# Performance work log

Measured on AMD Instinct MI355X. Metric: run time of the kernel, lower is better.

## Reference

```python
import jax, jax.numpy as jnp
import numpy as np

HEADS = 4
C_HEAD = 32


def setup_inputs() -> dict:
    key = jax.random.key(0)
    k1, k2, k3 = jax.random.split(key, 3)
    c_in = 256
    c_hid = HEADS * C_HEAD  # 128
    x = jax.random.normal(k1, (4, c_in, 64, 64), dtype=jnp.float32)
    # 1x1 conv weights stored as [out, in]
    w_qkv = jax.random.normal(k2, (3 * c_hid, c_in), dtype=jnp.float32) * (c_in ** -0.5)
    w_out = jax.random.normal(k3, (c_in, c_hid), dtype=jnp.float32) * (c_hid ** -0.5)
    b_out = jnp.zeros((c_in,), dtype=jnp.float32)
    return {"x": x, "w_qkv": w_qkv, "w_out": w_out, "b_out": b_out}


def reference(x, w_qkv, w_out, b_out):
    b, c, h, w = x.shape
    scale = C_HEAD ** -0.5
    # 1x1 conv == channel matmul
    qkv = jnp.einsum('bchw,oc->bohw', x, w_qkv)  # [b, 3*c_hid, h, w]
    q, k, v = jnp.split(qkv, 3, axis=1)
    # b (heads c_head) x y -> b heads c_head (x y)
    def to_heads(t):
        return t.reshape(b, HEADS, C_HEAD, h * w)
    q, k, v = to_heads(q) * scale, to_heads(k), to_heads(v)
    sim = jnp.einsum('bhci,bhcj->bhij', q, k)  # [b, heads, N, N]
    sim = sim - jax.lax.stop_gradient(jnp.max(sim, axis=-1, keepdims=True))
    attn = jax.nn.softmax(sim, axis=-1)
    out = jnp.einsum('bhij,bhcj->bhic', attn, v)  # [b, heads, N, c_head]
    # b h (x y) c -> b (h c) x y
    out = out.transpose(0, 1, 3, 2).reshape(b, HEADS * C_HEAD, h, w)
    out = jnp.einsum('bchw,oc->bohw', out, w_out) + b_out[None, :, None, None]
    return out
```

## Files before the change

### kernel.cpp

```cpp
#include <hip/hip_runtime.h>
#include <hip/hip_bf16.h>
#include <cstdint>
#include <cstddef>


#define NB 4
#define CIN 256
#define CHID 128
#define HEADS 4
#define CHEAD 32
#define NPOS 4096
#define BH 16
#define NTOT 16384
#define QKV_O 384
#define QSCALE_LOG2E 0.2550348229f

typedef float f32x2 __attribute__((ext_vector_type(2)));
typedef float f32x4 __attribute__((ext_vector_type(4)));
typedef float f32x16 __attribute__((ext_vector_type(16)));
typedef short s16x8 __attribute__((ext_vector_type(8)));

static __device__ __forceinline__ unsigned short f2bf(float f) {
    union { float f; unsigned u; } v; v.f = f;
    unsigned r = v.u + 0x7FFFu + ((v.u >> 16) & 1u);
    return (unsigned short)(r >> 16);
}

static __device__ __forceinline__ unsigned int pk2bf(float a, float b) {
    union { __hip_bfloat162 h; unsigned int u; } c;
    c.h = __float22bfloat162_rn(float2{a, b});
    return c.u;
}

static __device__ __forceinline__ void plswap(unsigned& a, unsigned& b) {
#if __has_builtin(__builtin_amdgcn_permlane32_swap)
    auto r = __builtin_amdgcn_permlane32_swap((int)a, (int)b, false, false);
    a = (unsigned)r[0];
    b = (unsigned)r[1];
#else
    int hh = (threadIdx.x >> 5) & 1;
    unsigned ta = (unsigned)__shfl_xor((int)a, 32);
    unsigned tb = (unsigned)__shfl_xor((int)b, 32);
    unsigned na = hh ? tb : a;
    unsigned nb = hh ? b : ta;
    a = na; b = nb;
#endif
}

static __device__ __forceinline__ s16x8 mk8(unsigned a, unsigned b, unsigned c, unsigned d) {
    union { unsigned u[4]; s16x8 v; } x;
    x.u[0] = a; x.u[1] = b; x.u[2] = c; x.u[3] = d;
    return x.v;
}

static __device__ __forceinline__ void async_cp16(const void* g, void* l) {
    __builtin_amdgcn_global_load_lds((const __attribute__((address_space(1))) unsigned int*)g,
                                     (__attribute__((address_space(3))) unsigned int*)l, 16, 0, 0);
}

#define MFMA32(a, b, c) __builtin_amdgcn_mfma_f32_32x32x16_bf16(a, b, c, 0, 0, 0)


#define PTILES (NB * (CIN / 64) * (NPOS / 64))
__global__ __launch_bounds__(256) void k_prep(const float* __restrict__ x,
                                              unsigned short* __restrict__ xT,
                                              const float* __restrict__ wqkv,
                                              const float* __restrict__ wout,
                                              unsigned short* __restrict__ wqkv_bf,
                                              unsigned short* __restrict__ wout_bf) {
    if (blockIdx.x >= PTILES) {
        int i = (blockIdx.x - PTILES) * 256 + threadIdx.x;
        if (i < QKV_O * CIN) wqkv_bf[i] = f2bf(wqkv[i]);
        if (i < CIN * CHID)  wout_bf[i] = f2bf(wout[i]);
        return;
    }
    __shared__ float tile[64][65];
    const int per_b = (CIN / 64) * (NPOS / 64);
    int b   = blockIdx.x / per_b;
    int rem = blockIdx.x % per_b;
    int ct = rem / (NPOS / 64);
    int nt = rem % (NPOS / 64);
    int c0 = ct * 64, n0 = nt * 64;
    int t = threadIdx.x;
    const float* xb = x + (size_t)b * CIN * NPOS;
#pragma unroll
    for (int it = 0; it < 4; ++it) {
        int c  = (t >> 4) + it * 16;
        int n4 = (t & 15) * 4;
        f32x4 v = *(const f32x4*)(xb + (size_t)(c0 + c) * NPOS + n0 + n4);
        tile[c][n4] = v[0]; tile[c][n4 + 1] = v[1];
        tile[c][n4 + 2] = v[2]; tile[c][n4 + 3] = v[3];
    }
    __syncthreads();
    unsigned short* xTb = xT + (size_t)b * NPOS * CIN;
#pragma unroll
    for (int it = 0; it < 2; ++it) {
        int slot = it * 256 + t;
        int n  = slot >> 3;
        int c8 = (slot & 7) * 8;
        union { unsigned short u[8]; s16x8 v; } pk;
#pragma unroll
        for (int r = 0; r < 8; ++r) pk.u[r] = f2bf(tile[c8 + r][n]);
        *(s16x8*)(xTb + (size_t)(n0 + n) * CIN + c0 + c8) = pk.v;
    }
}

__global__ __launch_bounds__(256, 4) void k_qkv(const unsigned short* __restrict__ wq,
                                                const unsigned short* __restrict__ xT,
                                                unsigned short* __restrict__ Q,
                                                unsigned short* __restrict__ K,
                                                unsigned short* __restrict__ V) {
    __shared__ __align__(16) unsigned char smem[2 * 12288];
    int mt = blockIdx.x % 3;
    int nt = blockIdx.x / 3;
    int wid = threadIdx.x >> 6, lane = threadIdx.x & 63;
    int quad = lane >> 4, low4 = lane & 15;
    int o0 = mt * 128, n0 = nt * 64;
    int lb = lane * 16;

    const unsigned short* srcA0 = wq + (size_t)(o0 + wid * 32 + low4) * CIN + quad * 8;
    const unsigned short* srcA1 = srcA0 + 16 * CIN;
    const unsigned short* srcB  = xT + (size_t)(n0 + wid * 16 + low4) * CIN + quad * 8;
    int dA0 = wid * 2048, dA1 = dA0 + 1024, dB = 8192 + wid * 1024;

    async_cp16(srcA0, smem + dA0 + lb);
    async_cp16(srcA1, smem + dA1 + lb);
    async_cp16(srcB,  smem + dB  + lb);
    __syncthreads();

    f32x4 acc[2][4] = {};
    for (int c = 0; c < 8; ++c) {
        if (c < 7) {
            unsigned char* nxt = smem + ((c + 1) & 1) * 12288;
            async_cp16(srcA0 + (c + 1) * 32, nxt + dA0 + lb);
            async_cp16(srcA1 + (c + 1) * 32, nxt + dA1 + lb);
            async_cp16(srcB  + (c + 1) * 32, nxt + dB  + lb);
        }
        const unsigned char* cur = smem + (c & 1) * 12288;
        s16x8 a0 = *(const s16x8*)(cur + wid * 2048 + lb);
        s16x8 a1 = *(const s16x8*)(cur + wid * 2048 + 1024 + lb);
#pragma unroll
        for (int j = 0; j < 4; ++j) {
            s16x8 bj = *(const s16x8*)(cur + 8192 + j * 1024 + lb);
            acc[0][j] = __builtin_amdgcn_mfma_f32_16x16x32_bf16(a0, bj, acc[0][j], 0, 0, 0);
            acc[1][j] = __builtin_amdgcn_mfma_f32_16x16x32_bf16(a1, bj, acc[1][j], 0, 0, 0);
        }
        __syncthreads();
    }

    int b = n0 >> 12, nbase = n0 & 4095;
    if (mt < 2) {
        unsigned short (*vtT)[136] = (unsigned short(*)[136])smem;
        float sc = (mt == 0) ? QSCALE_LOG2E : 1.0f;
#pragma unroll
        for (int i = 0; i < 2; ++i) {
            int ob = wid * 32 + i * 16 + quad * 4;
#pragma unroll
            for (int j = 0; j < 4; ++j) {
                int nl = j * 16 + low4;
                f32x4 v = acc[i][j];
                unsigned long long d =
                    (unsigned long long)pk2bf(v[0] * sc, v[1] * sc) |
                    ((unsigned long long)pk2bf(v[2] * sc, v[3] * sc) << 32);
                *(unsigned long long*)(&vtT[nl][ob]) = d;
            }
        }
        __syncthreads();
        if (mt == 0) {
#pragma unroll
            for (int it = 0; it < 4; ++it) {
                int slot = it * 256 + threadIdx.x;
                int n = slot >> 4, c16 = slot & 15;
                s16x8 val = *(const s16x8*)(&vtT[n][c16 * 8]);
                int o = c16 * 8, head = o >> 5, ch = o & 31;
                *(s16x8*)(Q + ((size_t)(b * 4 + head) * NPOS + nbase + n) * 32 + ch) = val;
            }
        } else {
#pragma unroll
            for (int it = 0; it < 4; ++it) {
                int slot = it * 256 + threadIdx.x;
                int c16 = slot >> 6, n = slot & 63;
                s16x8 val = *(const s16x8*)(&vtT[n][c16 * 8]);
                int o = c16 * 8, head = o >> 5, c0h = o & 31;
                int f = c0h >> 4, hh = (c0h >> 3) & 1;
                int nG = nbase + n;
                int bh = b * 4 + head;
                size_t addr = (((size_t)bh * 128 + (nG >> 5)) * 2 + f) * 512
                            + (size_t)((((hh << 5) | (nG & 31)) << 3));
                *(s16x8*)(K + addr) = val;
            }
        }
    } else {
        unsigned short* vt = (unsigned short*)smem;
#pragma unroll
        for (int i = 0; i < 2; ++i) {
            int ol = wid * 32 + i * 16 + quad * 4;
#pragma unroll
            for (int j = 0; j < 4; ++j) {
                int col = j * 16 + low4;
#pragma unroll
                for (int r = 0; r < 4; ++r) vt[(ol + r) * 80 + col] = f2bf(acc[i][j][r]);
            }
        }
        __syncthreads();
#pragma unroll
        for (int rep = 0; rep < 4; ++rep) {
            int idx = rep * 256 + threadIdx.x;
            int row = idx >> 3, c8 = idx & 7;
            s16x8 val = *(const s16x8*)(vt + row * 80 + c8 * 8);
            int head = row >> 5, ch = row & 31;
            int bh = b * 4 + head;
            int nstart = nbase + c8 * 8;
            int kc = nstart >> 4, hh = (nstart >> 3) & 1;
            *(s16x8*)(V + ((size_t)(bh * 256 + kc) * 64 + ((hh << 5) | ch)) * 8) = val;
        }
    }
}

__global__ __launch_bounds__(256, 4) void k_attn(const unsigned short* __restrict__ Q,
                                                 const unsigned short* __restrict__ K,
                                                 const unsigned short* __restrict__ V,
                                                 unsigned short* __restrict__ attnO) {
    __shared__ __align__(16) unsigned char smem[2 * 16384];
    int bh = blockIdx.x & 15;
    int qt = blockIdx.x >> 4;
    int wid = threadIdx.x >> 6;
    int lane = threadIdx.x & 63;
    int q5 = lane & 31, h = lane >> 5;
    int qg = wid & 1, kh = wid >> 1;
    int q0 = qt * 64 + qg * 32;
    int khk = kh * 2048;

    const unsigned short* Qp = Q + (size_t)bh * NPOS * 32;

    s16x8 bq0 = *(const s16x8*)(Qp + (size_t)(q0 + q5) * 32 + h * 8);
    s16x8 bq1 = *(const s16x8*)(Qp + (size_t)(q0 + q5) * 32 + 16 + h * 8);

    const unsigned short* pKf = K + (size_t)bh * 131072 + lane * 8;
    const unsigned short* pVf = V + (size_t)bh * 131072 + lane * 8;

    auto stage = [&](int bufi, int k0) {
        unsigned char* wb = smem + bufi * 16384 + kh * 8192;
        if (qg == 0) {
            const unsigned short* p = pKf + (size_t)(k0 >> 5) * 1024;
            async_cp16(p,        wb);
            async_cp16(p + 512,  wb + 1024);
            async_cp16(p + 1024, wb + 2048);
            async_cp16(p + 1536, wb + 3072);
        } else {
            const unsigned short* p = pVf + (size_t)(k0 >> 4) * 512;
            async_cp16(p,        wb + 4096);
            async_cp16(p + 512,  wb + 5120);
            async_cp16(p + 1024, wb + 6144);
            async_cp16(p + 1536, wb + 7168);
        }
    };

    f32x16 oT = {};
    f32x2 lacc0 = {0.0f, 0.0f}, lacc1 = {0.0f, 0.0f};
    const int lby = lane * 16;

    stage(0, khk);

#pragma unroll 1
    for (int it = 0; it < 32; ++it) {
        if (it + 1 < 32) {
            stage((it + 1) & 1, khk + (it + 1) * 64);
            asm volatile("s_waitcnt vmcnt(4)" ::: "memory");
        } else {
            asm volatile("s_waitcnt vmcnt(0)" ::: "memory");
        }
        asm volatile("s_barrier" ::: "memory");

        const unsigned char* kb = smem + (it & 1) * 16384 + kh * 8192;
#pragma unroll
        for (int t = 0; t < 2; ++t) {
            s16x8 ak0 = *(const s16x8*)(kb + t * 2048 + lby);
            s16x8 ak1 = *(const s16x8*)(kb + t * 2048 + 1024 + lby);
            f32x16 s = {};
            __builtin_amdgcn_s_setprio(1);
            s = MFMA32(ak0, bq0, s);
            s = MFMA32(ak1, bq1, s);
            __builtin_amdgcn_s_setprio(0);
            unsigned p[8];
#pragma unroll
            for (int i = 0; i < 8; ++i) {
                float e0 = __builtin_amdgcn_exp2f(s[2 * i]);
                float e1 = __builtin_amdgcn_exp2f(s[2 * i + 1]);
                f32x2 e = {e0, e1};
                if (i & 1) lacc0 += e;
                else       lacc1 += e;
                p[i] = pk2bf(e0, e1);
            }
            plswap(p[0], p[2]); plswap(p[1], p[3]);
            plswap(p[4], p[6]); plswap(p[5], p[7]);
            s16x8 bplo = mk8(p[0], p[1], p[2], p[3]);
            s16x8 bphi = mk8(p[4], p[5], p[6], p[7]);

            s16x8 av0 = *(const s16x8*)(kb + 4096 + (2 * t) * 1024 + lby);
            s16x8 av1 = *(const s16x8*)(kb + 4096 + (2 * t + 1) * 1024 + lby);
            __builtin_amdgcn_s_setprio(1);
            oT = MFMA32(av0, bplo, oT);
            oT = MFMA32(av1, bphi, oT);
            __builtin_amdgcn_s_setprio(0);
        }
        asm volatile("s_barrier" ::: "memory");
    }

    float lsum = lacc0[0] + lacc0[1] + lacc1[0] + lacc1[1];
    lsum += __shfl_xor(lsum, 32);

    if (kh) {
        float* area = (float*)(smem + qg * 4352);
#pragma unroll
        for (int j = 0; j < 4; ++j)
            *(f32x4*)(area + j * 256 + lane * 4) =
                f32x4{oT[4 * j], oT[4 * j + 1], oT[4 * j + 2], oT[4 * j + 3]};
        area[1024 + lane] = lsum;
    }
    __syncthreads();
    if (!kh) {
        const float* area = (const float*)(smem + qg * 4352);
        lsum += area[1024 + lane];
        float inv = 1.0f / lsum;
        int b = bh >> 2, head = bh & 3;
        int n = q0 + q5;
        unsigned short* base = attnO + ((size_t)(b * NPOS + n)) * CHID + head * 32 + 4 * h;
#pragma unroll
        for (int j = 0; j < 4; ++j) {
            f32x4 r = *(const f32x4*)(area + j * 256 + lane * 4);
            unsigned long long d =
                (unsigned long long)pk2bf((oT[4 * j] + r[0]) * inv, (oT[4 * j + 1] + r[1]) * inv) |
                ((unsigned long long)pk2bf((oT[4 * j + 2] + r[2]) * inv, (oT[4 * j + 3] + r[3]) * inv) << 32);
            *(unsigned long long*)(base + 8 * j) = d;
        }
    }
}

__global__ __launch_bounds__(256, 4) void k_out(const unsigned short* __restrict__ wo,
                                                const unsigned short* __restrict__ attnO,
                                                const float* __restrict__ bias,
                                                float* __restrict__ out) {
    __shared__ __align__(16) unsigned char smem[2 * 12288];
    int mt = blockIdx.x & 1;
    int nt = blockIdx.x >> 1;
    int wid = threadIdx.x >> 6, lane = threadIdx.x & 63;
    int quad = lane >> 4, low4 = lane & 15;
    int o0 = mt * 128, n0 = nt * 64;
    int lb = lane * 16;

    const unsigned short* srcA0 = wo + (size_t)(o0 + wid * 32 + low4) * CHID + quad * 8;
    const unsigned short* srcA1 = srcA0 + 16 * CHID;
    const unsigned short* srcB  = attnO + (size_t)(n0 + wid * 16 + low4) * CHID + quad * 8;
    int dA0 = wid * 2048, dA1 = dA0 + 1024, dB = 8192 + wid * 1024;

    async_cp16(srcA0, smem + dA0 + lb);
    async_cp16(srcA1, smem + dA1 + lb);
    async_cp16(srcB,  smem + dB  + lb);
    __syncthreads();

    f32x4 acc[2][4] = {};
    for (int c = 0; c < 4; ++c) {
        if (c < 3) {
            unsigned char* nxt = smem + ((c + 1) & 1) * 12288;
            async_cp16(srcA0 + (c + 1) * 32, nxt + dA0 + lb);
            async_cp16(srcA1 + (c + 1) * 32, nxt + dA1 + lb);
            async_cp16(srcB  + (c + 1) * 32, nxt + dB  + lb);
        }
        const unsigned char* cur = smem + (c & 1) * 12288;
        s16x8 a0 = *(const s16x8*)(cur + wid * 2048 + lb);
        s16x8 a1 = *(const s16x8*)(cur + wid * 2048 + 1024 + lb);
#pragma unroll
        for (int j = 0; j < 4; ++j) {
            s16x8 bj = *(const s16x8*)(cur + 8192 + j * 1024 + lb);
            acc[0][j] = __builtin_amdgcn_mfma_f32_16x16x32_bf16(a0, bj, acc[0][j], 0, 0, 0);
            acc[1][j] = __builtin_amdgcn_mfma_f32_16x16x32_bf16(a1, bj, acc[1][j], 0, 0, 0);
        }
        __syncthreads();
    }

    float (*larea)[68] = (float(*)[68])smem;
    int b = n0 >> 12, nb = n0 & 4095;
#pragma unroll
    for (int half = 0; half < 2; ++half) {
        if ((wid >> 1) == half) {
#pragma unroll
            for (int i = 0; i < 2; ++i) {
                int row = (wid & 1) * 32 + i * 16 + quad * 4;
                int o = o0 + half * 64 + row;
#pragma unroll
                for (int j = 0; j < 4; ++j) {
                    int nl = j * 16 + low4;
#pragma unroll
                    for (int r = 0; r < 4; ++r)
                        larea[row + r][nl] = acc[i][j][r] + bias[o + r];
                }
            }
        }
        __syncthreads();
#pragma unroll
        for (int it = 0; it < 4; ++it) {
            int slot = it * 256 + threadIdx.x;
            int row = slot >> 4, nn4 = (slot & 15) * 4;
            int o = o0 + half * 64 + row;
            f32x4 v = *(const f32x4*)(&larea[row][nn4]);
            *(f32x4*)(out + ((size_t)(b * CIN + o)) * NPOS + nb + nn4) = v;
        }
        __syncthreads();
    }
}

extern "C" void kernel_launch(void* const* d_in, const int* in_sizes, int n_in,
                              void* d_out, int out_size, void* d_ws, size_t ws_size,
                              hipStream_t stream) {
    const float* x    = (const float*)d_in[0];
    const float* wqkv = (const float*)d_in[1];
    const float* wout = (const float*)d_in[2];
    const float* bout = (const float*)d_in[3];
    float* out = (float*)d_out;

    unsigned short* Q       = (unsigned short*)d_ws;
    unsigned short* K       = Q + (size_t)BH * NPOS * 32;
    unsigned short* V       = K + (size_t)BH * NPOS * 32;
    unsigned short* attnO   = V + (size_t)BH * 32 * NPOS;
    unsigned short* xT      = attnO + (size_t)NTOT * CHID;
    unsigned short* wqkv_bf = xT + (size_t)NTOT * CIN;
    unsigned short* wout_bf = wqkv_bf + QKV_O * CIN;

    k_prep<<<PTILES + (QKV_O * CIN + 255) / 256, 256, 0, stream>>>(x, xT, wqkv, wout, wqkv_bf, wout_bf);
    k_qkv<<<3 * (NTOT / 64), 256, 0, stream>>>(wqkv_bf, xT, Q, K, V);
    k_attn<<<(NPOS / 64) * BH, 256, 0, stream>>>(Q, K, V, attnO);
    k_out<<<2 * (NTOT / 64), 256, 0, stream>>>(wout_bf, attnO, bout, out);
}
```

Before: 157.0 us.

## Fuse attention and output projection into one 1024-thread kernel per query tile

Merges the attention kernel and the output 1x1 conv kernel. Each 1024-thread block now processes all four heads of one batch for a 64-query tile. The normalized attention output stays in LDS as a bf16 tile, which feeds the wout MFMA projection directly. This removes the global attnO write and re-read and one kernel launch. In exchange each block uses 128KB of LDS, the grid shrinks to 256 blocks, and the launch bound (1024, 4) may squeeze the register budget and cause spills in the attention loop.

```diff
diff --git a/kernel.cpp b/kernel.cpp
--- a/kernel.cpp
+++ b/kernel.cpp
@@ -217,22 +217,24 @@
     }
 }
 
-__global__ __launch_bounds__(256, 4) void k_attn(const unsigned short* __restrict__ Q,
-                                                 const unsigned short* __restrict__ K,
-                                                 const unsigned short* __restrict__ V,
-                                                 unsigned short* __restrict__ attnO) {
-    __shared__ __align__(16) unsigned char smem[2 * 16384];
-    int bh = blockIdx.x & 15;
-    int qt = blockIdx.x >> 4;
+__global__ __launch_bounds__(1024, 4) void k_attn_out(const unsigned short* __restrict__ Q,
+                                                      const unsigned short* __restrict__ K,
+                                                      const unsigned short* __restrict__ V,
+                                                      const unsigned short* __restrict__ wo,
+                                                      const float* __restrict__ bias,
+                                                      float* __restrict__ out) {
+    __shared__ __align__(16) unsigned char smem[131072];
+    int b  = blockIdx.x & 3;
+    int qt = blockIdx.x >> 2;
     int wid = threadIdx.x >> 6;
     int lane = threadIdx.x & 63;
     int q5 = lane & 31, h = lane >> 5;
-    int qg = wid & 1, kh = wid >> 1;
+    int head = wid >> 2, kh = (wid >> 1) & 1, qg = wid & 1;
+    int bh = b * 4 + head;
     int q0 = qt * 64 + qg * 32;
     int khk = kh * 2048;
 
     const unsigned short* Qp = Q + (size_t)bh * NPOS * 32;
-
     s16x8 bq0 = *(const s16x8*)(Qp + (size_t)(q0 + q5) * 32 + h * 8);
     s16x8 bq1 = *(const s16x8*)(Qp + (size_t)(q0 + q5) * 32 + 16 + h * 8);
 
@@ -240,7 +242,7 @@
     const unsigned short* pVf = V + (size_t)bh * 131072 + lane * 8;
 
     auto stage = [&](int bufi, int k0) {
-        unsigned char* wb = smem + bufi * 16384 + kh * 8192;
+        unsigned char* wb = smem + bufi * 65536 + head * 16384 + kh * 8192;
         if (qg == 0) {
             const unsigned short* p = pKf + (size_t)(k0 >> 5) * 1024;
             async_cp16(p,        wb);
@@ -272,7 +274,7 @@
         }
         asm volatile("s_barrier" ::: "memory");
 
-        const unsigned char* kb = smem + (it & 1) * 16384 + kh * 8192;
+        const unsigned char* kb = smem + (it & 1) * 65536 + head * 16384 + kh * 8192;
 #pragma unroll
         for (int t = 0; t < 2; ++t) {
             s16x8 ak0 = *(const s16x8*)(kb + t * 2048 + lby);
@@ -310,8 +312,9 @@
     float lsum = lacc0[0] + lacc0[1] + lacc1[0] + lacc1[1];
     lsum += __shfl_xor(lsum, 32);
 
+    float* area = (float*)(smem + (head * 2 + qg) * 4352);
+    unsigned short* oblk = (unsigned short*)(smem + 98304);
     if (kh) {
-        float* area = (float*)(smem + qg * 4352);
 #pragma unroll
         for (int j = 0; j < 4; ++j)
             *(f32x4*)(area + j * 256 + lane * 4) =
@@ -320,93 +323,49 @@
     }
     __syncthreads();
     if (!kh) {
-        const float* area = (const float*)(smem + qg * 4352);
         lsum += area[1024 + lane];
         float inv = 1.0f / lsum;
-        int b = bh >> 2, head = bh & 3;
-        int n = q0 + q5;
-        unsigned short* base = attnO + ((size_t)(b * NPOS + n)) * CHID + head * 32 + 4 * h;
+        int n = qg * 32 + q5;
 #pragma unroll
         for (int j = 0; j < 4; ++j) {
             f32x4 r = *(const f32x4*)(area + j * 256 + lane * 4);
             unsigned long long d =
                 (unsigned long long)pk2bf((oT[4 * j] + r[0]) * inv, (oT[4 * j + 1] + r[1]) * inv) |
                 ((unsigned long long)pk2bf((oT[4 * j + 2] + r[2]) * inv, (oT[4 * j + 3] + r[3]) * inv) << 32);
-            *(unsigned long long*)(base + 8 * j) = d;
-        }
-    }
-}
-
-__global__ __launch_bounds__(256, 4) void k_out(const unsigned short* __restrict__ wo,
-                                                const unsigned short* __restrict__ attnO,
-                                                const float* __restrict__ bias,
-                                                float* __restrict__ out) {
-    __shared__ __align__(16) unsigned char smem[2 * 12288];
-    int mt = blockIdx.x & 1;
-    int nt = blockIdx.x >> 1;
-    int wid = threadIdx.x >> 6, lane = threadIdx.x & 63;
+            *(unsigned long long*)(oblk + n * 136 + head * 32 + 4 * h + 8 * j) = d;
+        }
+    }
+    __syncthreads();
+
     int quad = lane >> 4, low4 = lane & 15;
-    int o0 = mt * 128, n0 = nt * 64;
-    int lb = lane * 16;
-
-    const unsigned short* srcA0 = wo + (size_t)(o0 + wid * 32 + low4) * CHID + quad * 8;
-    const unsigned short* srcA1 = srcA0 + 16 * CHID;
-    const unsigned short* srcB  = attnO + (size_t)(n0 + wid * 16 + low4) * CHID + quad * 8;
-    int dA0 = wid * 2048, dA1 = dA0 + 1024, dB = 8192 + wid * 1024;
-
-    async_cp16(srcA0, smem + dA0 + lb);
-    async_cp16(srcA1, smem + dA1 + lb);
-    async_cp16(srcB,  smem + dB  + lb);
-    __syncthreads();
-
-    f32x4 acc[2][4] = {};
-    for (int c = 0; c < 4; ++c) {
-        if (c < 3) {
-            unsigned char* nxt = smem + ((c + 1) & 1) * 12288;
-            async_cp16(srcA0 + (c + 1) * 32, nxt + dA0 + lb);
-            async_cp16(srcA1 + (c + 1) * 32, nxt + dA1 + lb);
-            async_cp16(srcB  + (c + 1) * 32, nxt + dB  + lb);
-        }
-        const unsigned char* cur = smem + (c & 1) * 12288;
-        s16x8 a0 = *(const s16x8*)(cur + wid * 2048 + lb);
-        s16x8 a1 = *(const s16x8*)(cur + wid * 2048 + 1024 + lb);
+    const unsigned short* wrow = wo + (size_t)(wid * 16 + low4) * CHID + quad * 8;
+    s16x8 af[4];
+#pragma unroll
+    for (int c4 = 0; c4 < 4; ++c4) af[c4] = *(const s16x8*)(wrow + c4 * 32);
+    f32x4 acc[4] = {};
+#pragma unroll
+    for (int c4 = 0; c4 < 4; ++c4) {
 #pragma unroll
         for (int j = 0; j < 4; ++j) {
-            s16x8 bj = *(const s16x8*)(cur + 8192 + j * 1024 + lb);
-            acc[0][j] = __builtin_amdgcn_mfma_f32_16x16x32_bf16(a0, bj, acc[0][j], 0, 0, 0);
-            acc[1][j] = __builtin_amdgcn_mfma_f32_16x16x32_bf16(a1, bj, acc[1][j], 0, 0, 0);
-        }
-        __syncthreads();
-    }
-
-    float (*larea)[68] = (float(*)[68])smem;
-    int b = n0 >> 12, nb = n0 & 4095;
-#pragma unroll
-    for (int half = 0; half < 2; ++half) {
-        if ((wid >> 1) == half) {
-#pragma unroll
-            for (int i = 0; i < 2; ++i) {
-                int row = (wid & 1) * 32 + i * 16 + quad * 4;
-                int o = o0 + half * 64 + row;
-#pragma unroll
-                for (int j = 0; j < 4; ++j) {
-                    int nl = j * 16 + low4;
-#pragma unroll
-                    for (int r = 0; r < 4; ++r)
-                        larea[row + r][nl] = acc[i][j][r] + bias[o + r];
-                }
-            }
-        }
-        __syncthreads();
-#pragma unroll
-        for (int it = 0; it < 4; ++it) {
-            int slot = it * 256 + threadIdx.x;
-            int row = slot >> 4, nn4 = (slot & 15) * 4;
-            int o = o0 + half * 64 + row;
-            f32x4 v = *(const f32x4*)(&larea[row][nn4]);
-            *(f32x4*)(out + ((size_t)(b * CIN + o)) * NPOS + nb + nn4) = v;
-        }
-        __syncthreads();
+            s16x8 bj = *(const s16x8*)(oblk + (j * 16 + low4) * 136 + c4 * 32 + quad * 8);
+            acc[j] = __builtin_amdgcn_mfma_f32_16x16x32_bf16(af[c4], bj, acc[j], 0, 0, 0);
+        }
+    }
+
+    f32x4 bv = *(const f32x4*)(bias + wid * 16 + quad * 4);
+    float* larea = (float*)smem;
+#pragma unroll
+    for (int j = 0; j < 4; ++j)
+#pragma unroll
+        for (int r = 0; r < 4; ++r)
+            larea[(wid * 16 + quad * 4 + r) * 68 + j * 16 + low4] = acc[j][r] + bv[r];
+    __syncthreads();
+#pragma unroll
+    for (int it2 = 0; it2 < 4; ++it2) {
+        int slot = it2 * 1024 + threadIdx.x;
+        int row = slot >> 4, n4 = (slot & 15) * 4;
+        *(f32x4*)(out + ((size_t)(b * CIN + row)) * NPOS + qt * 64 + n4) =
+            *(const f32x4*)(larea + row * 68 + n4);
     }
 }
 
@@ -422,13 +381,11 @@
     unsigned short* Q       = (unsigned short*)d_ws;
     unsigned short* K       = Q + (size_t)BH * NPOS * 32;
     unsigned short* V       = K + (size_t)BH * NPOS * 32;
-    unsigned short* attnO   = V + (size_t)BH * 32 * NPOS;
-    unsigned short* xT      = attnO + (size_t)NTOT * CHID;
+    unsigned short* xT      = V + (size_t)BH * 32 * NPOS;
     unsigned short* wqkv_bf = xT + (size_t)NTOT * CIN;
     unsigned short* wout_bf = wqkv_bf + QKV_O * CIN;
 
     k_prep<<<PTILES + (QKV_O * CIN + 255) / 256, 256, 0, stream>>>(x, xT, wqkv, wout, wqkv_bf, wout_bf);
     k_qkv<<<3 * (NTOT / 64), 256, 0, stream>>>(wqkv_bf, xT, Q, K, V);
-    k_attn<<<(NPOS / 64) * BH, 256, 0, stream>>>(Q, K, V, attnO);
-    k_out<<<2 * (NTOT / 64), 256, 0, stream>>>(wout_bf, attnO, bout, out);
-}
+    k_attn_out<<<NB * (NPOS / 64), 1024, 0, stream>>>(Q, K, V, wout_bf, bout, out);
+}
```

After: 162.8 us. +3.7%, slower.

## Split attention keys across four waves per 32-query tile with per-wave staging

Applied to the files above, without the earlier changes.

Each block now handles 32 queries instead of 64. Its four waves each take a quarter of the keys, and each wave stages its own K/V chunk into a private LDS slice, so the per-iteration block barriers go away. The grid doubles, LDS per block halves and launch bounds allow 8 blocks per CU, all to raise occupancy. In exchange, each wave waits on its own loads with only single-buffering plus an issue-ahead after the LDS reads. The final reduction now merges three partial outputs through shared memory, and each K/V tile is loaded by twice as many blocks.

```diff
diff --git a/kernel.cpp b/kernel.cpp
--- a/kernel.cpp
+++ b/kernel.cpp
@@ -217,101 +217,86 @@
     }
 }
 
-__global__ __launch_bounds__(256, 4) void k_attn(const unsigned short* __restrict__ Q,
+__global__ __launch_bounds__(256, 8) void k_attn(const unsigned short* __restrict__ Q,
                                                  const unsigned short* __restrict__ K,
                                                  const unsigned short* __restrict__ V,
                                                  unsigned short* __restrict__ attnO) {
-    __shared__ __align__(16) unsigned char smem[2 * 16384];
+    __shared__ __align__(16) unsigned char smem[16384];
     int bh = blockIdx.x & 15;
     int qt = blockIdx.x >> 4;
     int wid = threadIdx.x >> 6;
     int lane = threadIdx.x & 63;
     int q5 = lane & 31, h = lane >> 5;
-    int qg = wid & 1, kh = wid >> 1;
-    int q0 = qt * 64 + qg * 32;
-    int khk = kh * 2048;
+    int q0 = qt * 32;
+    int k0 = wid * 1024;
 
     const unsigned short* Qp = Q + (size_t)bh * NPOS * 32;
-
     s16x8 bq0 = *(const s16x8*)(Qp + (size_t)(q0 + q5) * 32 + h * 8);
     s16x8 bq1 = *(const s16x8*)(Qp + (size_t)(q0 + q5) * 32 + 16 + h * 8);
 
     const unsigned short* pKf = K + (size_t)bh * 131072 + lane * 8;
     const unsigned short* pVf = V + (size_t)bh * 131072 + lane * 8;
-
-    auto stage = [&](int bufi, int k0) {
-        unsigned char* wb = smem + bufi * 16384 + kh * 8192;
-        if (qg == 0) {
-            const unsigned short* p = pKf + (size_t)(k0 >> 5) * 1024;
-            async_cp16(p,        wb);
-            async_cp16(p + 512,  wb + 1024);
-            async_cp16(p + 1024, wb + 2048);
-            async_cp16(p + 1536, wb + 3072);
-        } else {
-            const unsigned short* p = pVf + (size_t)(k0 >> 4) * 512;
-            async_cp16(p,        wb + 4096);
-            async_cp16(p + 512,  wb + 5120);
-            async_cp16(p + 1024, wb + 6144);
-            async_cp16(p + 1536, wb + 7168);
-        }
+    unsigned char* wb = smem + wid * 4096;
+    const int lby = lane * 16;
+
+    auto stage = [&](int kk) {
+        const unsigned short* pk = pKf + (size_t)(kk >> 5) * 1024;
+        const unsigned short* pv = pVf + (size_t)(kk >> 4) * 512;
+        async_cp16(pk,       wb);
+        async_cp16(pk + 512, wb + 1024);
+        async_cp16(pv,       wb + 2048);
+        async_cp16(pv + 512, wb + 3072);
     };
 
     f32x16 oT = {};
     f32x2 lacc0 = {0.0f, 0.0f}, lacc1 = {0.0f, 0.0f};
-    const int lby = lane * 16;
-
-    stage(0, khk);
+
+    stage(k0);
 
 #pragma unroll 1
     for (int it = 0; it < 32; ++it) {
-        if (it + 1 < 32) {
-            stage((it + 1) & 1, khk + (it + 1) * 64);
-            asm volatile("s_waitcnt vmcnt(4)" ::: "memory");
-        } else {
-            asm volatile("s_waitcnt vmcnt(0)" ::: "memory");
-        }
-        asm volatile("s_barrier" ::: "memory");
-
-        const unsigned char* kb = smem + (it & 1) * 16384 + kh * 8192;
-#pragma unroll
-        for (int t = 0; t < 2; ++t) {
-            s16x8 ak0 = *(const s16x8*)(kb + t * 2048 + lby);
-            s16x8 ak1 = *(const s16x8*)(kb + t * 2048 + 1024 + lby);
-            f32x16 s = {};
-            __builtin_amdgcn_s_setprio(1);
-            s = MFMA32(ak0, bq0, s);
-            s = MFMA32(ak1, bq1, s);
-            __builtin_amdgcn_s_setprio(0);
-            unsigned p[8];
-#pragma unroll
-            for (int i = 0; i < 8; ++i) {
-                float e0 = __builtin_amdgcn_exp2f(s[2 * i]);
-                float e1 = __builtin_amdgcn_exp2f(s[2 * i + 1]);
-                f32x2 e = {e0, e1};
-                if (i & 1) lacc0 += e;
-                else       lacc1 += e;
-                p[i] = pk2bf(e0, e1);
-            }
-            plswap(p[0], p[2]); plswap(p[1], p[3]);
-            plswap(p[4], p[6]); plswap(p[5], p[7]);
-            s16x8 bplo = mk8(p[0], p[1], p[2], p[3]);
-            s16x8 bphi = mk8(p[4], p[5], p[6], p[7]);
-
-            s16x8 av0 = *(const s16x8*)(kb + 4096 + (2 * t) * 1024 + lby);
-            s16x8 av1 = *(const s16x8*)(kb + 4096 + (2 * t + 1) * 1024 + lby);
-            __builtin_amdgcn_s_setprio(1);
-            oT = MFMA32(av0, bplo, oT);
-            oT = MFMA32(av1, bphi, oT);
-            __builtin_amdgcn_s_setprio(0);
-        }
-        asm volatile("s_barrier" ::: "memory");
+        asm volatile("s_waitcnt vmcnt(0)" ::: "memory");
+        s16x8 ak0 = *(const s16x8*)(wb + lby);
+        s16x8 ak1 = *(const s16x8*)(wb + 1024 + lby);
+        s16x8 av0 = *(const s16x8*)(wb + 2048 + lby);
+        s16x8 av1 = *(const s16x8*)(wb + 3072 + lby);
+        asm volatile("s_waitcnt lgkmcnt(0)" ::: "memory");
+        __builtin_amdgcn_sched_barrier(0);
+        if (it + 1 < 32) stage(k0 + (it + 1) * 32);
+        __builtin_amdgcn_sched_barrier(0);
+
+        f32x16 s = {};
+        __builtin_amdgcn_s_setprio(1);
+        s = MFMA32(ak0, bq0, s);
+        s = MFMA32(ak1, bq1, s);
+        __builtin_amdgcn_s_setprio(0);
+        unsigned p[8];
+#pragma unroll
+        for (int i = 0; i < 8; ++i) {
+            float e0 = __builtin_amdgcn_exp2f(s[2 * i]);
+            float e1 = __builtin_amdgcn_exp2f(s[2 * i + 1]);
+            f32x2 e = {e0, e1};
+            if (i & 1) lacc0 += e;
+            else       lacc1 += e;
+            p[i] = pk2bf(e0, e1);
+        }
+        plswap(p[0], p[2]); plswap(p[1], p[3]);
+        plswap(p[4], p[6]); plswap(p[5], p[7]);
+        s16x8 bplo = mk8(p[0], p[1], p[2], p[3]);
+        s16x8 bphi = mk8(p[4], p[5], p[6], p[7]);
+        __builtin_amdgcn_s_setprio(1);
+        oT = MFMA32(av0, bplo, oT);
+        oT = MFMA32(av1, bphi, oT);
+        __builtin_amdgcn_s_setprio(0);
     }
 
     float lsum = lacc0[0] + lacc0[1] + lacc1[0] + lacc1[1];
     lsum += __shfl_xor(lsum, 32);
 
-    if (kh) {
-        float* area = (float*)(smem + qg * 4352);
+    __syncthreads();
+
+    if (wid) {
+        float* area = (float*)(smem + (wid - 1) * 4352);
 #pragma unroll
         for (int j = 0; j < 4; ++j)
             *(f32x4*)(area + j * 256 + lane * 4) =
@@ -319,19 +304,25 @@
         area[1024 + lane] = lsum;
     }
     __syncthreads();
-    if (!kh) {
-        const float* area = (const float*)(smem + qg * 4352);
-        lsum += area[1024 + lane];
+    if (!wid) {
+        const float* a0 = (const float*)(smem);
+        const float* a1 = (const float*)(smem + 4352);
+        const float* a2 = (const float*)(smem + 8704);
+        lsum += a0[1024 + lane] + a1[1024 + lane] + a2[1024 + lane];
         float inv = 1.0f / lsum;
         int b = bh >> 2, head = bh & 3;
         int n = q0 + q5;
         unsigned short* base = attnO + ((size_t)(b * NPOS + n)) * CHID + head * 32 + 4 * h;
 #pragma unroll
         for (int j = 0; j < 4; ++j) {
-            f32x4 r = *(const f32x4*)(area + j * 256 + lane * 4);
+            f32x4 r0 = *(const f32x4*)(a0 + j * 256 + lane * 4);
+            f32x4 r1 = *(const f32x4*)(a1 + j * 256 + lane * 4);
+            f32x4 r2 = *(const f32x4*)(a2 + j * 256 + lane * 4);
             unsigned long long d =
-                (unsigned long long)pk2bf((oT[4 * j] + r[0]) * inv, (oT[4 * j + 1] + r[1]) * inv) |
-                ((unsigned long long)pk2bf((oT[4 * j + 2] + r[2]) * inv, (oT[4 * j + 3] + r[3]) * inv) << 32);
+                (unsigned long long)pk2bf((oT[4 * j] + r0[0] + r1[0] + r2[0]) * inv,
+                                          (oT[4 * j + 1] + r0[1] + r1[1] + r2[1]) * inv) |
+                ((unsigned long long)pk2bf((oT[4 * j + 2] + r0[2] + r1[2] + r2[2]) * inv,
+                                           (oT[4 * j + 3] + r0[3] + r1[3] + r2[3]) * inv) << 32);
             *(unsigned long long*)(base + 8 * j) = d;
         }
     }
@@ -429,6 +420,6 @@
 
     k_prep<<<PTILES + (QKV_O * CIN + 255) / 256, 256, 0, stream>>>(x, xT, wqkv, wout, wqkv_bf, wout_bf);
     k_qkv<<<3 * (NTOT / 64), 256, 0, stream>>>(wqkv_bf, xT, Q, K, V);
-    k_attn<<<(NPOS / 64) * BH, 256, 0, stream>>>(Q, K, V, attnO);
+    k_attn<<<(NPOS / 32) * BH, 256, 0, stream>>>(Q, K, V, attnO);
     k_out<<<2 * (NTOT / 64), 256, 0, stream>>>(wout_bf, attnO, bout, out);
 }
```

Result: slower. 160.2 us (+2.0%).
